# Kernel tuning notes

Measured on AMD Instinct MI355X. Metric: run time of the kernel, lower is better.

The kernel has to match this reference:

```python
import jax, jax.numpy as jnp
import numpy as np

V, E, H, L, HID, T, B = 50257, 512, 8, 8, 1365, 1024, 2
HD = E // H
EPS = 1e-5


def setup_inputs() -> dict:
    key = jax.random.key(0)
    ks = jax.random.split(key, 9)
    s = 0.02
    def nrm(k, shape):
        return jax.random.normal(k, shape, jnp.float32) * s
    return {
        "idx": jax.random.randint(ks[0], (B, T), 0, V),
        "W_emb": nrm(ks[1], (V, E)),          # tied tok_emb / lm head
        "pos_emb": nrm(ks[2], (T, E)),
        "ln1_s": jnp.ones((L, E)), "ln1_b": jnp.zeros((L, E)),
        "qkv_w": nrm(ks[3], (L, E, 3 * E)),
        "proj_w": nrm(ks[4], (L, E, E)),
        "ln2_s": jnp.ones((L, E)), "ln2_b": jnp.zeros((L, E)),
        "gate_w": nrm(ks[5], (L, E, HID)),
        "up_w": nrm(ks[6], (L, E, HID)),
        "down_w": nrm(ks[7], (L, HID, E)),
        "lnf_s": jnp.ones((E,)), "lnf_b": jnp.zeros((E,)),
    }


def _ln(x, s, b):
    m = x.mean(-1, keepdims=True)
    v = ((x - m) ** 2).mean(-1, keepdims=True)
    return (x - m) * jax.lax.rsqrt(v + EPS) * s + b


def _forward(idx, W_emb, pos_emb, ln1_s, ln1_b, qkv_w, proj_w,
             ln2_s, ln2_b, gate_w, up_w, down_w, lnf_s, lnf_b):
    x = W_emb[idx] + pos_emb[None, :, :]  # [B,T,E]
    pos = jnp.arange(T)
    # faithful to source: ALiBi bias uses |i-j|, added before causal mask
    dist = jnp.abs(pos[None, :] - pos[:, None]).astype(jnp.float32)  # [T,T]
    slopes = (1.0 / 2.0 ** (8.0 * jnp.arange(1, H + 1, dtype=jnp.float32) / H))
    alibi = slopes[:, None, None] * dist[None]  # [H,T,T]
    causal = jnp.tril(jnp.ones((T, T), bool))
    scale = 1.0 / np.sqrt(HD)

    def block(x, p):
        l1s, l1b, qkvw, pw, l2s, l2b, gw, uw, dw = p
        h = _ln(x, l1s, l1b)
        qkv = h @ qkvw  # [B,T,3E]
        q, k, v = jnp.split(qkv, 3, axis=-1)
        q = q.reshape(B, T, H, HD).transpose(0, 2, 1, 3)
        k = k.reshape(B, T, H, HD).transpose(0, 2, 1, 3)
        v = v.reshape(B, T, H, HD).transpose(0, 2, 1, 3)
        att = jnp.einsum('bhqd,bhkd->bhqk', q, k) * scale + alibi[None]
        att = jnp.where(causal, att, -jnp.inf)
        att = jax.nn.softmax(att, axis=-1)
        o = jnp.einsum('bhqk,bhkd->bhqd', att, v)
        o = o.transpose(0, 2, 1, 3).reshape(B, T, E)
        x = x + o @ pw
        h = _ln(x, l2s, l2b)
        g = h @ gw
        x = x + (g * jax.nn.sigmoid(g) * (h @ uw)) @ dw  # SwiGLU
        return x, None

    x, _ = jax.lax.scan(block, x, (ln1_s, ln1_b, qkv_w, proj_w,
                                   ln2_s, ln2_b, gate_w, up_w, down_w))
    x = _ln(x, lnf_s, lnf_b)
    return x @ W_emb.T  # tied head -> [B,T,V]


def reference(idx, W_emb, pos_emb, ln1_s, ln1_b, qkv_w, proj_w,
              ln2_s, ln2_b, gate_w, up_w, down_w, lnf_s, lnf_b):
    return _forward(idx, W_emb, pos_emb, ln1_s, ln1_b, qkv_w, proj_w,
                    ln2_s, ln2_b, gate_w, up_w, down_w, lnf_s, lnf_b)
```

## Files before the change

kernel.cpp:

```cpp
#include <hip/hip_runtime.h>
#include <hip/hip_bf16.h>
#include <math.h>

#define V_SZ 50257
#define V_PAD 50304
#define E_SZ 512
#define H_N 8
#define L_N 8
#define HID_SZ 1365
#define HID_PAD 1408
#define T_SZ 1024
#define B_SZ 2
#define HD_SZ 64
#define ROWS (B_SZ * T_SZ)

typedef short bf16x8 __attribute__((ext_vector_type(8)));
typedef float f32x4 __attribute__((ext_vector_type(4)));
typedef float f32x16 __attribute__((ext_vector_type(16)));

__global__ __launch_bounds__(128) void embed_kernel(
    const int* __restrict__ idx, const float* __restrict__ W,
    const float* __restrict__ P, float* __restrict__ x,
    float* __restrict__ stats) {
  const int bt = blockIdx.x;
  const int t = bt & (T_SZ - 1);
  const int id = idx[bt];
  const int e = threadIdx.x * 4;
  float4 w = *(const float4*)(W + (size_t)id * E_SZ + e);
  float4 p = *(const float4*)(P + (size_t)t * E_SZ + e);
  float4 r;
  r.x = w.x + p.x; r.y = w.y + p.y; r.z = w.z + p.z; r.w = w.w + p.w;
  *(float4*)(x + (size_t)bt * E_SZ + e) = r;
  float s = r.x + r.y + r.z + r.w;
  float q = r.x * r.x + r.y * r.y + r.z * r.z + r.w * r.w;
#pragma unroll
  for (int o = 32; o; o >>= 1) { s += __shfl_xor(s, o); q += __shfl_xor(q, o); }
  __shared__ float sr[4];
  if ((threadIdx.x & 63) == 0) {
    sr[(threadIdx.x >> 6) * 2] = s;
    sr[(threadIdx.x >> 6) * 2 + 1] = q;
  }
  __syncthreads();
  if (threadIdx.x < 16) {
    float a = (threadIdx.x == 0) ? sr[0] + sr[2] : 0.f;
    float b2 = (threadIdx.x == 0) ? sr[1] + sr[3] : 0.f;
    float* st = stats + (size_t)bt * 32 + threadIdx.x * 2;
    st[0] = a; st[1] = b2;
  }
}

__global__ __launch_bounds__(256) void ln_from_stats(
    const float* __restrict__ x, const float* __restrict__ stats,
    const float* __restrict__ gamma, const float* __restrict__ beta,
    __hip_bfloat16* __restrict__ out) {
  const int row = blockIdx.x;
  const int tid = threadIdx.x;
  const float* sp = stats + (size_t)row * 32;
  float sum = 0.f, ssq = 0.f;
#pragma unroll
  for (int i = 0; i < 8; ++i) {
    float4 v = ((const float4*)sp)[i];
    sum += v.x + v.z; ssq += v.y + v.w;
  }
  const float mean = sum * (1.f / 512.f);
  const float var = ssq * (1.f / 512.f) - mean * mean;
  const float rstd = rsqrtf(var + 1e-5f);
  const float2 v = *(const float2*)(x + (size_t)row * E_SZ + tid * 2);
  const float2 sv = *(const float2*)(gamma + tid * 2);
  const float2 bv = *(const float2*)(beta + tid * 2);
  __hip_bfloat162 ov;
  ov.x = __float2bfloat16((v.x - mean) * rstd * sv.x + bv.x);
  ov.y = __float2bfloat16((v.y - mean) * rstd * sv.y + bv.y);
  *(__hip_bfloat162*)(out + (size_t)row * E_SZ + tid * 2) = ov;
}

__global__ __launch_bounds__(256) void convert_wemb(
    const float* __restrict__ W, __hip_bfloat16* __restrict__ Wb) {
  const int tid = blockIdx.x * 256 + threadIdx.x;
  const int row = tid >> 6;
  const int c = (tid & 63) * 8;
  union { __hip_bfloat16 h[8]; int4 v; } u;
  if (row < V_SZ) {
    const float* p = W + (size_t)row * E_SZ + c;
#pragma unroll
    for (int j = 0; j < 8; ++j) u.h[j] = __float2bfloat16(p[j]);
  } else {
#pragma unroll
    for (int j = 0; j < 8; ++j) u.h[j] = __float2bfloat16(0.f);
  }
  *(int4*)(Wb + (size_t)row * E_SZ + c) = u.v;
}

__global__ __launch_bounds__(256) void transp_convert(
    const float* __restrict__ in, __hip_bfloat16* __restrict__ out,
    int K, int N, int Kpad, int Npad) {
  __shared__ float tile[32][33];
  const int l = blockIdx.z;
  in  += (size_t)l * K * N;
  out += (size_t)l * Npad * Kpad;
  const int tx = threadIdx.x & 31, ty = threadIdx.x >> 5;
  const int n0 = blockIdx.x * 32, k0 = blockIdx.y * 32;
#pragma unroll
  for (int i = 0; i < 4; ++i) {
    const int k = k0 + ty + i * 8, n = n0 + tx;
    tile[ty + i * 8][tx] = (k < K && n < N) ? in[(size_t)k * N + n] : 0.f;
  }
  __syncthreads();
#pragma unroll
  for (int i = 0; i < 4; ++i) {
    const int n = n0 + ty + i * 8, kk = k0 + tx;
    out[(size_t)n * Kpad + kk] = __float2bfloat16(tile[tx][ty + i * 8]);
  }
}

__global__ __launch_bounds__(256) void gu_prep(
    const float* __restrict__ gate, const float* __restrict__ up,
    __hip_bfloat16* __restrict__ outw) {
  __shared__ float tile[32][33];
  const int l = blockIdx.z;
  const int c0 = blockIdx.x * 32, k0 = blockIdx.y * 32;
  const int tx = threadIdx.x & 31, ty = threadIdx.x >> 5;
#pragma unroll
  for (int role = 0; role < 2; ++role) {
    const float* src = (role ? up : gate) + (size_t)l * E_SZ * HID_SZ;
#pragma unroll
    for (int i = 0; i < 4; ++i) {
      const int k = k0 + ty + i * 8, c = c0 + tx;
      tile[ty + i * 8][tx] = (c < HID_SZ) ? src[(size_t)k * HID_SZ + c] : 0.f;
    }
    __syncthreads();
#pragma unroll
    for (int i = 0; i < 4; ++i) {
      const int c = c0 + ty + i * 8, kk = k0 + tx;
      const int n = ((c >> 4) << 5) | (role << 4) | (c & 15);
      outw[((size_t)l * 2816 + n) * E_SZ + kk] = __float2bfloat16(tile[tx][ty + i * 8]);
    }
    __syncthreads();
  }
}

template <int EPI>
__global__ __launch_bounds__(256) void gemm64ln(
    const float* __restrict__ X, const __hip_bfloat16* __restrict__ B,
    void* __restrict__ Cv, const float* __restrict__ stats,
    const float* __restrict__ gamma, const float* __restrict__ beta,
    int N, int K) {
  __shared__ char lds[16384];
  __shared__ float gb[1024];
  const int tid = threadIdx.x, lane = tid & 63, w = tid >> 6;
  const int wr = w >> 1, wc = w & 1;
  const int m0 = blockIdx.y * 64, n0 = blockIdx.x * 64;
  const size_t SB = (size_t)K * 2;
  char* As = lds;
  char* Bs = lds + 8192;
  const char* Bb = (const char*)B + (size_t)n0 * SB;
  f32x4 acc[2][2] = {};
  const int lrow = lane >> 3;
  const int schunk = ((lane & 7) ^ lrow) * 16;
  const int kb = (lane >> 4) * 16;

  for (int i = tid; i < 512; i += 256) { gb[i] = gamma[i]; gb[512 + i] = beta[i]; }

  const int arow = tid >> 2, acol = (tid & 3) * 16;
  const int achunk0 = acol >> 3;
  const int akey = arow & 7;
  float mean, rstd;
  {
    const float* sp = stats + (size_t)(m0 + arow) * 32;
    float sum = 0.f, ssq = 0.f;
#pragma unroll
    for (int i = 0; i < 8; ++i) {
      float4 v = ((const float4*)sp)[i];
      sum += v.x + v.z; ssq += v.y + v.w;
    }
    mean = sum * (1.f / 512.f);
    const float var = ssq * (1.f / 512.f) - mean * mean;
    rstd = rsqrtf(var + 1e-5f);
  }
  const float* Xrow = X + (size_t)(m0 + arow) * K;
  __syncthreads();

  for (int k0 = 0; k0 < K; k0 += 64) {
#pragma unroll
    for (int i = 0; i < 2; ++i) {
      const int row = w * 8 + 32 * i + lrow;
      const char* gbp = Bb + (size_t)row * SB + k0 * 2 + schunk;
      __builtin_amdgcn_global_load_lds(
          (const __attribute__((address_space(1))) unsigned int*)gbp,
          (__attribute__((address_space(3))) unsigned int*)(Bs + w * 1024 + i * 4096),
          16, 0, 0);
    }
    {
      float xf[16];
      const float* xs = Xrow + k0 + acol;
      *(float4*)&xf[0]  = ((const float4*)xs)[0];
      *(float4*)&xf[4]  = ((const float4*)xs)[1];
      *(float4*)&xf[8]  = ((const float4*)xs)[2];
      *(float4*)&xf[12] = ((const float4*)xs)[3];
      union { __hip_bfloat16 h[16]; int4 v[2]; } pk;
#pragma unroll
      for (int jj = 0; jj < 16; ++jj) {
        const int col = k0 + acol + jj;
        pk.h[jj] = __float2bfloat16((xf[jj] - mean) * rstd * gb[col] + gb[512 + col]);
      }
      *(int4*)(As + arow * 128 + (((achunk0 + 0) ^ akey) * 16)) = pk.v[0];
      *(int4*)(As + arow * 128 + (((achunk0 + 1) ^ akey) * 16)) = pk.v[1];
    }
    __syncthreads();
    bf16x8 a[2][2], bb[2][2];
#pragma unroll
    for (int i = 0; i < 2; ++i) {
      const int ra = wr * 32 + i * 16 + (lane & 15);
      const int rb = wc * 32 + i * 16 + (lane & 15);
#pragma unroll
      for (int ks = 0; ks < 2; ++ks) {
        a[i][ks]  = *(const bf16x8*)(As + ra * 128 + ((ks * 64 + kb) ^ ((ra & 7) << 4)));
        bb[i][ks] = *(const bf16x8*)(Bs + rb * 128 + ((ks * 64 + kb) ^ ((rb & 7) << 4)));
      }
    }
#pragma unroll
    for (int ks = 0; ks < 2; ++ks)
#pragma unroll
      for (int i = 0; i < 2; ++i)
#pragma unroll
        for (int j = 0; j < 2; ++j)
          acc[i][j] = __builtin_amdgcn_mfma_f32_16x16x32_bf16(a[i][ks], bb[j][ks], acc[i][j], 0, 0, 0);
    __syncthreads();
  }

  const int cr = (lane >> 4) * 4, ccol = lane & 15;
  if (EPI == 3) {
    __hip_bfloat16* G = (__hip_bfloat16*)Cv;
    const int cg = (n0 >> 1) + wc * 16 + ccol;
#pragma unroll
    for (int i = 0; i < 2; ++i) {
#pragma unroll
      for (int rr = 0; rr < 4; ++rr) {
        const int m = m0 + wr * 32 + i * 16 + cr + rr;
        const float gv = acc[i][0][rr];
        const float uv = acc[i][1][rr];
        const float val = gv / (1.f + __expf(-gv)) * uv;
        G[(size_t)m * HID_PAD + cg] = __float2bfloat16(val);
      }
    }
  } else {
    __hip_bfloat16* O = (__hip_bfloat16*)Cv;
#pragma unroll
    for (int i = 0; i < 2; ++i)
#pragma unroll
      for (int j = 0; j < 2; ++j) {
        const int n = n0 + wc * 32 + j * 16 + ccol;
#pragma unroll
        for (int rr = 0; rr < 4; ++rr) {
          const int m = m0 + wr * 32 + i * 16 + cr + rr;
          O[(size_t)m * N + n] = __float2bfloat16(acc[i][j][rr]);
        }
      }
  }
}

__global__ __launch_bounds__(256) void gemm64(
    const __hip_bfloat16* __restrict__ A, const __hip_bfloat16* __restrict__ B,
    float* __restrict__ C, const float* __restrict__ R,
    float* __restrict__ stats, int N, int K) {
  __shared__ char lds[49152];
  const int tid = threadIdx.x, lane = tid & 63, w = tid >> 6;
  const int wr = w >> 1, wc = w & 1;
  const int m0 = blockIdx.y * 64, n0 = blockIdx.x * 64;
  const size_t SA = (size_t)K * 2;
  const char* Ab = (const char*)A + (size_t)m0 * SA;
  const char* Bb = (const char*)B + (size_t)n0 * SA;
  f32x4 acc[2][2] = {};
  const int lrow = lane >> 3;
  const int schunk = ((lane & 7) ^ lrow) * 16;
  const int kb = (lane >> 4) * 16;

  auto STAGE = [&](int buf, int t) {
    char* As = lds + buf * 16384;
    char* Bs = As + 8192;
    const int k0b = t * 128;
#pragma unroll
    for (int i = 0; i < 2; ++i) {
      const int row = w * 8 + 32 * i + lrow;
      const char* ga = Ab + (size_t)row * SA + k0b + schunk;
      __builtin_amdgcn_global_load_lds(
          (const __attribute__((address_space(1))) unsigned int*)ga,
          (__attribute__((address_space(3))) unsigned int*)(As + w * 1024 + i * 4096),
          16, 0, 0);
      const char* gbp = Bb + (size_t)row * SA + k0b + schunk;
      __builtin_amdgcn_global_load_lds(
          (const __attribute__((address_space(1))) unsigned int*)gbp,
          (__attribute__((address_space(3))) unsigned int*)(Bs + w * 1024 + i * 4096),
          16, 0, 0);
    }
  };

  const int NT = K >> 6;
  STAGE(0, 0);
  if (NT > 1) STAGE(1, 1);
  for (int t = 0; t < NT; ++t) {
    if (t + 2 < NT) {
      STAGE((t + 2) % 3, t + 2);
      asm volatile("s_waitcnt vmcnt(8)" ::: "memory");
    } else if (t + 1 < NT) {
      asm volatile("s_waitcnt vmcnt(4)" ::: "memory");
    } else {
      asm volatile("s_waitcnt vmcnt(0)" ::: "memory");
    }
    __builtin_amdgcn_s_barrier();
    asm volatile("" ::: "memory");
    const char* As = lds + (t % 3) * 16384;
    const char* Bs = As + 8192;
    bf16x8 a[2][2], bb[2][2];
#pragma unroll
    for (int i = 0; i < 2; ++i) {
      const int ra = wr * 32 + i * 16 + (lane & 15);
      const int rb = wc * 32 + i * 16 + (lane & 15);
#pragma unroll
      for (int ks = 0; ks < 2; ++ks) {
        a[i][ks]  = *(const bf16x8*)(As + ra * 128 + ((ks * 64 + kb) ^ ((ra & 7) << 4)));
        bb[i][ks] = *(const bf16x8*)(Bs + rb * 128 + ((ks * 64 + kb) ^ ((rb & 7) << 4)));
      }
    }
    __builtin_amdgcn_s_setprio(1);
#pragma unroll
    for (int ks = 0; ks < 2; ++ks)
#pragma unroll
      for (int i = 0; i < 2; ++i)
#pragma unroll
        for (int j = 0; j < 2; ++j)
          acc[i][j] = __builtin_amdgcn_mfma_f32_16x16x32_bf16(a[i][ks], bb[j][ks], acc[i][j], 0, 0, 0);
    __builtin_amdgcn_s_setprio(0);
    asm volatile("" ::: "memory");
    __builtin_amdgcn_s_barrier();
    asm volatile("" ::: "memory");
  }

  const int cr = (lane >> 4) * 4, ccol = lane & 15;
  float vv[2][2][4];
#pragma unroll
  for (int i = 0; i < 2; ++i)
#pragma unroll
    for (int j = 0; j < 2; ++j) {
      const int n = n0 + wc * 32 + j * 16 + ccol;
#pragma unroll
      for (int rr = 0; rr < 4; ++rr) {
        const int m = m0 + wr * 32 + i * 16 + cr + rr;
        const float v = acc[i][j][rr] + R[(size_t)m * N + n];
        vv[i][j][rr] = v;
        C[(size_t)m * N + n] = v;
      }
    }
  const int slice = blockIdx.x * 2 + wc;
#pragma unroll
  for (int i = 0; i < 2; ++i) {
#pragma unroll
    for (int rr = 0; rr < 4; ++rr) {
      float s = vv[i][0][rr] + vv[i][1][rr];
      float q = vv[i][0][rr] * vv[i][0][rr] + vv[i][1][rr] * vv[i][1][rr];
#pragma unroll
      for (int o = 1; o < 16; o <<= 1) { s += __shfl_xor(s, o); q += __shfl_xor(q, o); }
      if ((lane & 15) == 0) {
        const int m = m0 + wr * 32 + i * 16 + cr + rr;
        float* st = stats + (size_t)m * 32 + slice * 2;
        st[0] = s; st[1] = q;
      }
    }
  }
}

__global__ __launch_bounds__(256) void head_gemm(
    const __hip_bfloat16* __restrict__ A, const __hip_bfloat16* __restrict__ B,
    float* __restrict__ C, int N, int K) {
  __shared__ char lds[49152];
  const int tid = threadIdx.x;
  const int lane = tid & 63, w = tid >> 6;
  const int wr = w >> 1, wc = w & 1;
  const int nwg = gridDim.x * gridDim.y;
  const int id = blockIdx.y * gridDim.x + blockIdx.x;
  const int work = (id & 7) * (nwg >> 3) + (id >> 3);
  const int bx = work >> 4, by = work & 15;
  const int m0 = by * 128, n0 = bx * 128;
  const size_t SA = (size_t)K * 2;

  f32x4 acc[4][4] = {};
  const char* Ab = (const char*)A + (size_t)m0 * SA;
  const char* Bb = (const char*)B + (size_t)n0 * SA;

  const int srow = tid >> 2, schnk = tid & 3;

  auto STAGE = [&](int buf, int t) {
    char* As = lds + buf * 16384;
    char* Bs = As + 8192;
    const int k0b = t * 64;
#pragma unroll
    for (int i = 0; i < 2; ++i) {
      const int r = srow + i * 64;
      const int gc = (schnk ^ (r & 3)) * 16;
      const char* ga = Ab + (size_t)r * SA + k0b + gc;
      __builtin_amdgcn_global_load_lds(
          (const __attribute__((address_space(1))) unsigned int*)ga,
          (__attribute__((address_space(3))) unsigned int*)(As + i * 4096 + tid * 16),
          16, 0, 0);
      const char* gbp = Bb + (size_t)r * SA + k0b + gc;
      __builtin_amdgcn_global_load_lds(
          (const __attribute__((address_space(1))) unsigned int*)gbp,
          (__attribute__((address_space(3))) unsigned int*)(Bs + i * 4096 + tid * 16),
          16, 0, 0);
    }
  };

  const int kb = lane >> 4;
  STAGE(0, 0);
  STAGE(1, 1);
#pragma unroll
  for (int t = 0; t < 16; ++t) {
    if (t + 2 < 16) STAGE((t + 2) % 3, t + 2);
    if (t <= 13)      asm volatile("s_waitcnt vmcnt(8)" ::: "memory");
    else if (t == 14) asm volatile("s_waitcnt vmcnt(4)" ::: "memory");
    else              asm volatile("s_waitcnt vmcnt(0)" ::: "memory");
    __builtin_amdgcn_s_barrier();
    asm volatile("" ::: "memory");
    const char* As = lds + (t % 3) * 16384;
    const char* Bs = As + 8192;
    bf16x8 a[4], b[4];
#pragma unroll
    for (int i = 0; i < 4; ++i) {
      const int ra = wr * 64 + i * 16 + (lane & 15);
      const int rb = wc * 64 + i * 16 + (lane & 15);
      a[i] = *(const bf16x8*)(As + ra * 64 + ((kb ^ (ra & 3)) * 16));
      b[i] = *(const bf16x8*)(Bs + rb * 64 + ((kb ^ (rb & 3)) * 16));
    }
    __builtin_amdgcn_s_setprio(1);
#pragma unroll
    for (int i = 0; i < 4; ++i)
#pragma unroll
      for (int j = 0; j < 4; ++j)
        acc[i][j] = __builtin_amdgcn_mfma_f32_16x16x32_bf16(a[i], b[j], acc[i][j], 0, 0, 0);
    __builtin_amdgcn_s_setprio(0);
    asm volatile("" ::: "memory");
    __builtin_amdgcn_s_barrier();
    asm volatile("" ::: "memory");
  }

  const int cr = (lane >> 4) * 4, ccol = lane & 15;
#pragma unroll
  for (int i = 0; i < 4; ++i) {
#pragma unroll
    for (int j = 0; j < 4; ++j) {
      const int n = n0 + wc * 64 + j * 16 + ccol;
      if (n >= N) continue;
#pragma unroll
      for (int rr = 0; rr < 4; ++rr) {
        const int m = m0 + wr * 64 + i * 16 + cr + rr;
        C[(size_t)m * N + n] = acc[i][j][rr];
      }
    }
  }
}

__global__ __launch_bounds__(256, 1) void attn_mfma_kernel(
    const __hip_bfloat16* __restrict__ qkv, __hip_bfloat16* __restrict__ o) {
  const int bid = blockIdx.x;
  const int qb = bid & 15;
  const int h = (bid >> 4) & 7;
  const int b = bid >> 7;
  const int tid = threadIdx.x;
  const int w = tid >> 6, lane = tid & 63;
  const int g = w >> 1;
  const int wq = w & 1;
  const int l31 = lane & 31, hi = lane >> 5;
  const int q0w = qb * 64 + 32 * wq;
  const float slope = exp2f(-(float)(h + 1));
  const int rowstride = 3 * E_SZ;
  const int nch = qb + 1;
  const int niter = (nch + 1) >> 1;

  __shared__ char lds[32768];
  char* Kb = lds + g * 16384;
  char* Vb = Kb + 8192;

  bf16x8 qf[4];
  {
    const __hip_bfloat16* qrow = qkv + (size_t)(b * T_SZ + q0w + l31) * rowstride + h * HD_SZ;
#pragma unroll
    for (int dblk = 0; dblk < 4; ++dblk)
      qf[dblk] = *(const bf16x8*)(qrow + dblk * 16 + hi * 8);
  }

  f32x16 oacc[2][2] = {};
  float m[2] = {-INFINITY, -INFINITY}, lsum[2] = {0.f, 0.f};

  int4 kreg[4];
  int4 va[2], vb[2];
  const int ltid = tid & 127;
  const int jK = ltid >> 1, halfK = ltid & 1;
  const int jqV = ltid >> 2, qtV = ltid & 3;
  const int j0V = jqV * 2, d0V = qtV * 16;

  auto ISSUE = [&](int c) {
    const __hip_bfloat16* srcK = qkv + (size_t)(b * T_SZ + c * 64 + jK) * rowstride + E_SZ + h * HD_SZ + halfK * 32;
    kreg[0] = ((const int4*)srcK)[0]; kreg[1] = ((const int4*)srcK)[1];
    kreg[2] = ((const int4*)srcK)[2]; kreg[3] = ((const int4*)srcK)[3];
    const __hip_bfloat16* srcV = qkv + (size_t)(b * T_SZ + c * 64 + j0V) * rowstride + 2 * E_SZ + h * HD_SZ + d0V;
    va[0] = ((const int4*)srcV)[0]; va[1] = ((const int4*)srcV)[1];
    vb[0] = ((const int4*)(srcV + rowstride))[0]; vb[1] = ((const int4*)(srcV + rowstride))[1];
  };
  auto WRITE = [&]() {
#pragma unroll
    for (int u2 = 0; u2 < 4; ++u2) {
      const int d0 = halfK * 32 + u2 * 8;
      *(int4*)(Kb + jK * 128 + ((2 * d0) ^ ((jK & 7) << 4))) = kreg[u2];
    }
    union { int4 v[2]; unsigned short us[16]; } ua, ub;
    ua.v[0] = va[0]; ua.v[1] = va[1];
    ub.v[0] = vb[0]; ub.v[1] = vb[1];
#pragma unroll
    for (int e = 0; e < 16; ++e) {
      const int d = d0V + e;
      const unsigned wv = (unsigned)ua.us[e] | ((unsigned)ub.us[e] << 16);
      *(unsigned*)(Vb + d * 128 + ((2 * j0V) ^ ((d & 7) << 4))) = wv;
    }
  };

  if (g < nch) ISSUE(g);
  for (int it = 0; it < niter; ++it) {
    const int c = 2 * it + g;
    const bool act = c < nch;
    if (act) WRITE();
    __syncthreads();
    if (c + 2 < nch) ISSUE(c + 2);
    if (act) {
#pragma unroll
      for (int s = 0; s < 2; ++s) {
        const int j0 = c * 64 + 32 * s;
        if (j0 <= q0w + 31) {
          const int st = s;
          f32x16 sacc = {};
          const int jrow = 32 * s + l31;
          __builtin_amdgcn_s_setprio(1);
#pragma unroll
          for (int dblk = 0; dblk < 4; ++dblk) {
            bf16x8 kf = *(const bf16x8*)(Kb + jrow * 128 + ((dblk * 32 + hi * 16) ^ ((jrow & 7) << 4)));
            sacc = __builtin_amdgcn_mfma_f32_32x32x16_bf16(kf, qf[dblk], sacc, 0, 0, 0);
          }
          __builtin_amdgcn_s_setprio(0);
          const int qg = q0w + l31;
          float p[16];
          float tmax = -1e30f;
#pragma unroll
          for (int r = 0; r < 16; ++r) {
            const int jg = j0 + (r & 3) + 8 * (r >> 2) + 4 * hi;
            const float sv = (jg > qg) ? -1e9f : (sacc[r] * 0.125f + slope * (float)(qg - jg));
            p[r] = sv;
            tmax = fmaxf(tmax, sv);
          }
          tmax = fmaxf(tmax, __shfl_xor(tmax, 32));
          if (!__all(tmax <= m[st] + 8.f)) {
            const float mnew = fmaxf(m[st], tmax);
            const float corr = __expf(m[st] - mnew);
            lsum[st] *= corr;
#pragma unroll
            for (int dt = 0; dt < 2; ++dt)
#pragma unroll
              for (int r = 0; r < 16; ++r) oacc[st][dt][r] *= corr;
            m[st] = mnew;
          }
          float tsum = 0.f;
#pragma unroll
          for (int r = 0; r < 16; ++r) {
            p[r] = __expf(p[r] - m[st]);
            tsum += p[r];
          }
          tsum += __shfl_xor(tsum, 32);
          lsum[st] += tsum;
          unsigned wds[8];
#pragma unroll
          for (int k = 0; k < 8; ++k) {
            union { __hip_bfloat16 hh[2]; unsigned u; } pk_;
            pk_.hh[0] = __float2bfloat16(p[2 * k]);
            pk_.hh[1] = __float2bfloat16(p[2 * k + 1]);
            wds[k] = pk_.u;
          }
          bf16x8 pfrag[2];
#pragma unroll
          for (int jb = 0; jb < 2; ++jb) {
            const unsigned w0 = wds[4 * jb + 0], w1 = wds[4 * jb + 1];
            const unsigned w2 = wds[4 * jb + 2], w3 = wds[4 * jb + 3];
            const unsigned x2 = (unsigned)__shfl_xor((int)w2, 32);
            const unsigned x3 = (unsigned)__shfl_xor((int)w3, 32);
            const unsigned x0 = (unsigned)__shfl_xor((int)w0, 32);
            const unsigned x1 = (unsigned)__shfl_xor((int)w1, 32);
            union { unsigned u[4]; bf16x8 v; } pf;
            pf.u[0] = hi ? x2 : w0;
            pf.u[1] = hi ? x3 : w1;
            pf.u[2] = hi ? w2 : x0;
            pf.u[3] = hi ? w3 : x1;
            pfrag[jb] = pf.v;
          }
          __builtin_amdgcn_s_setprio(1);
#pragma unroll
          for (int dt = 0; dt < 2; ++dt) {
            const int row = dt * 32 + l31;
#pragma unroll
            for (int jb = 0; jb < 2; ++jb) {
              bf16x8 vt = *(const bf16x8*)(Vb + row * 128 + ((s * 64 + jb * 32 + hi * 16) ^ ((row & 7) << 4)));
              oacc[st][dt] = __builtin_amdgcn_mfma_f32_32x32x16_bf16(vt, pfrag[jb], oacc[st][dt], 0, 0, 0);
            }
          }
          __builtin_amdgcn_s_setprio(0);
        }
      }
    }
    __syncthreads();
  }

  float mW, lW;
  float Ow[2][16];
  if (g < nch) {
    const float mm = fmaxf(m[0], m[1]);
    const float a = __expf(m[0] - mm), b2 = __expf(m[1] - mm);
    mW = mm;
    lW = lsum[0] * a + lsum[1] * b2;
#pragma unroll
    for (int dt = 0; dt < 2; ++dt)
#pragma unroll
      for (int r = 0; r < 16; ++r)
        Ow[dt][r] = oacc[0][dt][r] * a + oacc[1][dt][r] * b2;
  } else {
    mW = -INFINITY; lW = 0.f;
#pragma unroll
    for (int dt = 0; dt < 2; ++dt)
#pragma unroll
      for (int r = 0; r < 16; ++r) Ow[dt][r] = 0.f;
  }

  float* Obuf = (float*)lds + wq * 2048;
  float* mlb  = (float*)lds + 4096 + wq * 64;
  __syncthreads();
  if (g == 1) {
#pragma unroll
    for (int dt = 0; dt < 2; ++dt)
#pragma unroll
      for (int r = 0; r < 16; ++r)
        Obuf[lane * 32 + dt * 16 + r] = Ow[dt][r];
    if (hi == 0) { mlb[l31 * 2] = mW; mlb[l31 * 2 + 1] = lW; }
  }
  __syncthreads();
  if (g == 0) {
    const float m1 = mlb[l31 * 2], l1 = mlb[l31 * 2 + 1];
    const float mmF = fmaxf(mW, m1);
    const float wA = __expf(mW - mmF), wB = __expf(m1 - mmF);
    const float inv = 1.f / (lW * wA + l1 * wB);
    __hip_bfloat16* orow = o + (size_t)(b * T_SZ + q0w + l31) * E_SZ + h * HD_SZ;
#pragma unroll
    for (int dt = 0; dt < 2; ++dt) {
#pragma unroll
      for (int gq = 0; gq < 4; ++gq) {
        union { __hip_bfloat16 hh[4]; short4 v; } ov;
#pragma unroll
        for (int e = 0; e < 4; ++e) {
          const int r = 4 * gq + e;
          const float o1 = Obuf[lane * 32 + dt * 16 + r];
          ov.hh[e] = __float2bfloat16((Ow[dt][r] * wA + o1 * wB) * inv);
        }
        *(short4*)(orow + dt * 32 + 4 * hi + 8 * gq) = ov.v;
      }
    }
  }
}

extern "C" void kernel_launch(void* const* d_in, const int* in_sizes, int n_in,
                              void* d_out, int out_size, void* d_ws, size_t ws_size,
                              hipStream_t stream) {
  const int* idx      = (const int*)d_in[0];
  const float* W_emb  = (const float*)d_in[1];
  const float* pos    = (const float*)d_in[2];
  const float* ln1_s  = (const float*)d_in[3];
  const float* ln1_b  = (const float*)d_in[4];
  const float* qkv_w  = (const float*)d_in[5];
  const float* proj_w = (const float*)d_in[6];
  const float* ln2_s  = (const float*)d_in[7];
  const float* ln2_b  = (const float*)d_in[8];
  const float* gate_w = (const float*)d_in[9];
  const float* up_w   = (const float*)d_in[10];
  const float* down_w = (const float*)d_in[11];
  const float* lnf_s  = (const float*)d_in[12];
  const float* lnf_b  = (const float*)d_in[13];
  float* out = (float*)d_out;

  char* p = (char*)d_ws;
  auto alloc = [&](size_t bytes) { char* q = p; p += (bytes + 255) & ~255ULL; return q; };
  float* x      = (float*)alloc((size_t)ROWS * E_SZ * 4);
  float* statsA = (float*)alloc((size_t)ROWS * 32 * 4);
  float* statsB = (float*)alloc((size_t)ROWS * 32 * 4);
  __hip_bfloat16* qkv_bf = (__hip_bfloat16*)alloc((size_t)ROWS * 3 * E_SZ * 2);
  __hip_bfloat16* h_bf  = (__hip_bfloat16*)alloc((size_t)ROWS * E_SZ * 2);
  __hip_bfloat16* o_bf  = (__hip_bfloat16*)alloc((size_t)ROWS * E_SZ * 2);
  __hip_bfloat16* g_bf  = (__hip_bfloat16*)alloc((size_t)ROWS * HID_PAD * 2);
  __hip_bfloat16* Wb    = (__hip_bfloat16*)alloc((size_t)V_PAD * E_SZ * 2);
  __hip_bfloat16* qkvwb = (__hip_bfloat16*)alloc((size_t)L_N * 3 * E_SZ * E_SZ * 2);
  __hip_bfloat16* projwb= (__hip_bfloat16*)alloc((size_t)L_N * E_SZ * E_SZ * 2);
  __hip_bfloat16* guwb  = (__hip_bfloat16*)alloc((size_t)L_N * 2816 * E_SZ * 2);
  __hip_bfloat16* downwb= (__hip_bfloat16*)alloc((size_t)L_N * E_SZ * HID_PAD * 2);

  convert_wemb<<<(V_PAD * E_SZ / 8 + 255) / 256, 256, 0, stream>>>(W_emb, Wb);
  transp_convert<<<dim3(3 * E_SZ / 32, E_SZ / 32, L_N), 256, 0, stream>>>(
      qkv_w, qkvwb, E_SZ, 3 * E_SZ, E_SZ, 3 * E_SZ);
  transp_convert<<<dim3(E_SZ / 32, E_SZ / 32, L_N), 256, 0, stream>>>(
      proj_w, projwb, E_SZ, E_SZ, E_SZ, E_SZ);
  gu_prep<<<dim3(HID_PAD / 32, E_SZ / 32, L_N), 256, 0, stream>>>(gate_w, up_w, guwb);
  transp_convert<<<dim3(E_SZ / 32, HID_PAD / 32, L_N), 256, 0, stream>>>(
      down_w, downwb, HID_SZ, E_SZ, HID_PAD, E_SZ);

  embed_kernel<<<ROWS, 128, 0, stream>>>(idx, W_emb, pos, x, statsA);

  for (int l = 0; l < L_N; ++l) {
    gemm64ln<1><<<dim3(3 * E_SZ / 64, ROWS / 64), 256, 0, stream>>>(
        x, qkvwb + (size_t)l * 3 * E_SZ * E_SZ, qkv_bf, statsA,
        ln1_s + l * E_SZ, ln1_b + l * E_SZ, 3 * E_SZ, E_SZ);
    attn_mfma_kernel<<<B_SZ * H_N * (T_SZ / 64), 256, 0, stream>>>(qkv_bf, o_bf);
    gemm64<<<dim3(E_SZ / 64, ROWS / 64), 256, 0, stream>>>(
        o_bf, projwb + (size_t)l * E_SZ * E_SZ, x, x, statsB, E_SZ, E_SZ);
    gemm64ln<3><<<dim3(2816 / 64, ROWS / 64), 256, 0, stream>>>(
        x, guwb + (size_t)l * 2816 * E_SZ, g_bf, statsB,
        ln2_s + l * E_SZ, ln2_b + l * E_SZ, 2816, E_SZ);
    gemm64<<<dim3(E_SZ / 64, ROWS / 64), 256, 0, stream>>>(
        g_bf, downwb + (size_t)l * E_SZ * HID_PAD, x, x, statsA, E_SZ, HID_PAD);
  }

  ln_from_stats<<<ROWS, 256, 0, stream>>>(x, statsA, lnf_s, lnf_b, h_bf);
  head_gemm<<<dim3(V_PAD / 128, 16), 256, 0, stream>>>(h_bf, Wb, out, V_SZ, E_SZ);
}
```

Before: 1.070 ms.

## Triple-buffer LDS pipeline in LN-fused GEMM with prefetched A/B tiles

Rewrites the K loop of the layernorm-fused GEMM as a three-stage software pipeline. B tiles are staged into LDS two iterations ahead, and the X rows are prefetched into registers one step further ahead. Explicit waitcnt and s_barrier calls replace the per-iteration __syncthreads, and MFMA issue priority is raised with s_setprio. This is meant to hide global-load latency behind MFMA work. In exchange, LDS rises to 48KB per block, which can lower occupancy, and the trip count is hardcoded to K=512.

```diff
diff --git a/kernel.cpp b/kernel.cpp
--- a/kernel.cpp
+++ b/kernel.cpp
@@ -145,14 +145,12 @@
     void* __restrict__ Cv, const float* __restrict__ stats,
     const float* __restrict__ gamma, const float* __restrict__ beta,
     int N, int K) {
-  __shared__ char lds[16384];
+  __shared__ char lds[49152];
   __shared__ float gb[1024];
   const int tid = threadIdx.x, lane = tid & 63, w = tid >> 6;
   const int wr = w >> 1, wc = w & 1;
   const int m0 = blockIdx.y * 64, n0 = blockIdx.x * 64;
   const size_t SB = (size_t)K * 2;
-  char* As = lds;
-  char* Bs = lds + 8192;
   const char* Bb = (const char*)B + (size_t)n0 * SB;
   f32x4 acc[2][2] = {};
   const int lrow = lane >> 3;
@@ -180,33 +178,52 @@
   const float* Xrow = X + (size_t)(m0 + arow) * K;
   __syncthreads();
 
-  for (int k0 = 0; k0 < K; k0 += 64) {
+  float xr[16];
+  auto XLOAD = [&](int t) {
+    const float* xs = Xrow + t * 64 + acol;
+    *(float4*)&xr[0]  = ((const float4*)xs)[0];
+    *(float4*)&xr[4]  = ((const float4*)xs)[1];
+    *(float4*)&xr[8]  = ((const float4*)xs)[2];
+    *(float4*)&xr[12] = ((const float4*)xs)[3];
+  };
+  auto STAGEB = [&](int buf, int t) {
+    char* Bs = lds + buf * 16384 + 8192;
 #pragma unroll
     for (int i = 0; i < 2; ++i) {
       const int row = w * 8 + 32 * i + lrow;
-      const char* gbp = Bb + (size_t)row * SB + k0 * 2 + schunk;
+      const char* gbp = Bb + (size_t)row * SB + t * 128 + schunk;
       __builtin_amdgcn_global_load_lds(
           (const __attribute__((address_space(1))) unsigned int*)gbp,
           (__attribute__((address_space(3))) unsigned int*)(Bs + w * 1024 + i * 4096),
           16, 0, 0);
     }
-    {
-      float xf[16];
-      const float* xs = Xrow + k0 + acol;
-      *(float4*)&xf[0]  = ((const float4*)xs)[0];
-      *(float4*)&xf[4]  = ((const float4*)xs)[1];
-      *(float4*)&xf[8]  = ((const float4*)xs)[2];
-      *(float4*)&xf[12] = ((const float4*)xs)[3];
-      union { __hip_bfloat16 h[16]; int4 v[2]; } pk;
-#pragma unroll
-      for (int jj = 0; jj < 16; ++jj) {
-        const int col = k0 + acol + jj;
-        pk.h[jj] = __float2bfloat16((xf[jj] - mean) * rstd * gb[col] + gb[512 + col]);
-      }
-      *(int4*)(As + arow * 128 + (((achunk0 + 0) ^ akey) * 16)) = pk.v[0];
-      *(int4*)(As + arow * 128 + (((achunk0 + 1) ^ akey) * 16)) = pk.v[1];
-    }
-    __syncthreads();
+  };
+  auto WRITEA = [&](int buf, int t) {
+    char* As = lds + buf * 16384;
+    union { __hip_bfloat16 h[16]; int4 v[2]; } pk;
+#pragma unroll
+    for (int jj = 0; jj < 16; ++jj) {
+      const int col = t * 64 + acol + jj;
+      pk.h[jj] = __float2bfloat16((xr[jj] - mean) * rstd * gb[col] + gb[512 + col]);
+    }
+    *(int4*)(As + arow * 128 + (((achunk0 + 0) ^ akey) * 16)) = pk.v[0];
+    *(int4*)(As + arow * 128 + (((achunk0 + 1) ^ akey) * 16)) = pk.v[1];
+  };
+
+  const int NT = 8;
+  XLOAD(0); STAGEB(0, 0); WRITEA(0, 0);
+  XLOAD(1); STAGEB(1, 1); WRITEA(1, 1);
+  XLOAD(2);
+#pragma unroll
+  for (int t = 0; t < NT; ++t) {
+    if (t + 2 < NT) { STAGEB((t + 2) % 3, t + 2); WRITEA((t + 2) % 3, t + 2); }
+    if (t + 3 < NT) XLOAD(t + 3);
+    if (t < NT - 1) asm volatile("s_waitcnt vmcnt(6) lgkmcnt(0)" ::: "memory");
+    else            asm volatile("s_waitcnt vmcnt(0) lgkmcnt(0)" ::: "memory");
+    __builtin_amdgcn_s_barrier();
+    asm volatile("" ::: "memory");
+    const char* As = lds + (t % 3) * 16384;
+    const char* Bs = As + 8192;
     bf16x8 a[2][2], bb[2][2];
 #pragma unroll
     for (int i = 0; i < 2; ++i) {
@@ -218,6 +235,7 @@
         bb[i][ks] = *(const bf16x8*)(Bs + rb * 128 + ((ks * 64 + kb) ^ ((rb & 7) << 4)));
       }
     }
+    __builtin_amdgcn_s_setprio(1);
 #pragma unroll
     for (int ks = 0; ks < 2; ++ks)
 #pragma unroll
@@ -225,7 +243,10 @@
 #pragma unroll
         for (int j = 0; j < 2; ++j)
           acc[i][j] = __builtin_amdgcn_mfma_f32_16x16x32_bf16(a[i][ks], bb[j][ks], acc[i][j], 0, 0, 0);
-    __syncthreads();
+    __builtin_amdgcn_s_setprio(0);
+    asm volatile("" ::: "memory");
+    __builtin_amdgcn_s_barrier();
+    asm volatile("" ::: "memory");
   }
 
   const int cr = (lane >> 4) * 4, ccol = lane & 15;
```

Measured after the change: 1.015 ms (median of 2 runs). 1.05x faster.
